# Performance work log

Measured on AMD Instinct MI355X. Metric: run time of the kernel, lower is better.

## Reference

```python
import jax, jax.numpy as jnp
import numpy as np

N, L, D = 2, 1024, 4544
H, DKV = 71, 64
ROPE_BASE = 10000.0


def _rope_tables(seq_len, head_dim, dtype):
    inv_freq = 1.0 / (ROPE_BASE ** (jnp.arange(0, head_dim, 2, dtype=jnp.float32) / head_dim))
    t = jnp.arange(seq_len, dtype=jnp.float32)
    freqs = jnp.outer(t, inv_freq)               # [L, Dkv/2]
    emb = jnp.concatenate([freqs, freqs], -1)    # [L, Dkv]
    return jnp.cos(emb).astype(dtype), jnp.sin(emb).astype(dtype)


def _apply_rotary(x, cos, sin):
    # x: [..., L, Dkv]; cos/sin: [L, Dkv] broadcast
    left, right = jnp.split(x, 2, axis=-1)
    rotated = jnp.concatenate([-right, left], axis=-1)
    return x * cos + rotated * sin


def setup_inputs() -> dict:
    key = jax.random.key(0)
    k1, k2, k3 = jax.random.split(key, 3)
    hidden_states = jax.random.normal(k1, (N, L, D), dtype=jnp.float32)
    w_qkv = jax.random.normal(k2, (D + 2 * DKV, D), dtype=jnp.float32) * (1.0 / np.sqrt(D))
    w_dense = jax.random.normal(k3, (D, D), dtype=jnp.float32) * (1.0 / np.sqrt(D))
    return {"hidden_states": hidden_states, "w_qkv": w_qkv, "w_dense": w_dense}


def reference(hidden_states, w_qkv, w_dense):
    n, l, d = hidden_states.shape
    # fused QKV projection -> [N, L, H+2, Dkv]
    fused = (hidden_states @ w_qkv.T).reshape(n, l, H + 2, DKV)
    q = fused[:, :, :-2, :]          # [N, L, H, Dkv]
    k = fused[:, :, -2, :]           # [N, L, Dkv] (single MQA kv head)
    v = fused[:, :, -1, :]           # [N, L, Dkv]

    cos, sin = _rope_tables(l, DKV, hidden_states.dtype)
    q = _apply_rotary(q, cos[:, None, :], sin[:, None, :])   # broadcast over heads
    k = _apply_rotary(k, cos, sin)

    scale = 1.0 / np.sqrt(DKV)
    # scores: [N, H, Lq, Lk]; kv head broadcast across all H query heads
    scores = jnp.einsum('nqhd,nkd->nhqk', q, k) * scale
    causal = jnp.tril(jnp.ones((l, l), dtype=bool))
    scores = jnp.where(causal, scores, jnp.finfo(scores.dtype).min)
    attn = jax.nn.softmax(scores, axis=-1)
    out = jnp.einsum('nhqk,nkd->nqhd', attn, v)              # [N, L, H, Dkv]
    out = out.reshape(n, l, H * DKV)
    return out @ w_dense.T
```

## Files before the change

### kernel.cpp

```cpp
#include <hip/hip_runtime.h>

typedef unsigned short u16;
typedef __attribute__((ext_vector_type(8))) short short8;
typedef __attribute__((ext_vector_type(4))) float floatx4;

__device__ __forceinline__ u16 f2bf(float f) {
    union { float f; unsigned int u; } v;
    v.f = f;
    unsigned int u = v.u;
    return (u16)((u + 0x7FFFu + ((u >> 16) & 1u)) >> 16);
}

__device__ __forceinline__ void cvt8_f32_bf16(const float* __restrict__ p, u16* dst) {
    const float4 x = *(const float4*)p;
    const float4 y = *(const float4*)(p + 4);
    short8 s;
    s[0] = (short)f2bf(x.x); s[1] = (short)f2bf(x.y);
    s[2] = (short)f2bf(x.z); s[3] = (short)f2bf(x.w);
    s[4] = (short)f2bf(y.x); s[5] = (short)f2bf(y.y);
    s[6] = (short)f2bf(y.z); s[7] = (short)f2bf(y.w);
    *(short8*)dst = s;
}

__device__ __forceinline__ void gld_lds16(const u16* g, u16* l) {
    __builtin_amdgcn_global_load_lds(
        (const __attribute__((address_space(1))) void*)g,
        (__attribute__((address_space(3))) void*)l,
        16, 0, 0);
}

__global__ __launch_bounds__(256) void cvt3_kernel(
    const float* __restrict__ a, u16* __restrict__ oa, long na,
    const float* __restrict__ b, u16* __restrict__ ob, long nb,
    const float* __restrict__ c, u16* __restrict__ oc, long nc) {
    const float* in; u16* out; long n;
    if (blockIdx.y == 0)      { in = a; out = oa; n = na; }
    else if (blockIdx.y == 1) { in = b; out = ob; n = nb; }
    else                      { in = c; out = oc; n = nc; }
    const long i = ((long)blockIdx.x * 256 + threadIdx.x) * 8;
    if (i >= n) return;
    cvt8_f32_bf16(in + i, out + i);
}


#define GEMM8P_PROLOGUE()                                                      \
    const int t    = threadIdx.x;                                              \
    const int w    = t >> 6;                                                   \
    const int lane = t & 63;                                                   \
    const int quad = lane >> 4;                                                \
    const int l16  = lane & 15;                                                \
    const int sw   = lane & 7;                                                 \
    const int nwg  = gridDim.x;                                                \
    const int qq = nwg >> 3, rr = nwg & 7;                                     \
    const int xcd = blockIdx.x & 7, idx = blockIdx.x >> 3;                     \
    const int wgid = (xcd < rr ? xcd * (qq + 1)                                \
                               : rr * (qq + 1) + (xcd - rr) * qq) + idx;       \
    const int m0 = (wgid / nt) * 256;                                          \
    const int n0 = (wgid % nt) * 256;                                          \
    const int wm = (w >> 2) * 128;                                             \
    const int wn = (w & 3) * 64;                                               \
    const int trow = t >> 3;                                                   \
    const int scol = ((t & 7) ^ (trow & 7)) * 8;                               \
    const long Kl = K;                                                         \
    const u16* Asrc = A + (long)(m0 + trow) * Kl + scol;                       \
    auto stageA = [&](int jt, int h, int b) {                                  \
        _Pragma("unroll")                                                      \
        for (int i = 0; i < 2; i++) {                                          \
            const u16* src = Asrc + (long)(h * 128 + i * 64) * Kl + (long)jt * 64; \
            u16* dst = &aLds[b][0] + h * 8192 + i * 4096 + t * 8;              \
            gld_lds16(src, dst);                                               \
        }                                                                      \
    };                                                                         \
    auto stageB = [&](int jt, int h, int b) {                                  \
        _Pragma("unroll")                                                      \
        for (int i = 0; i < 2; i++) {                                          \
            int rb = n0 + h * 128 + i * 64 + trow;                             \
            if (rb > N - 1) rb = N - 1;                                        \
            const u16* src = B + (long)rb * Kl + scol + (long)jt * 64;         \
            u16* dst = &bLds[b][0] + h * 8192 + i * 4096 + t * 8;              \
            gld_lds16(src, dst);                                               \
        }                                                                      \
    };                                                                         \
    floatx4 acc[8][4];                                                         \
    const floatx4 zf4 = {0.f, 0.f, 0.f, 0.f};                                  \
    _Pragma("unroll")                                                          \
    for (int i = 0; i < 8; i++)                                                \
        _Pragma("unroll")                                                      \
        for (int j = 0; j < 4; j++) acc[i][j] = zf4;                           \
                          \
    stageA(0, 0, 0); stageA(0, 1, 0);                                          \
    stageB(0, 0, 0); stageB(0, 1, 0);                                          \
    stageB(1, 0, 1); stageB(1, 1, 1);                                          \
    asm volatile("s_waitcnt vmcnt(4)" ::: "memory");                           \
    __builtin_amdgcn_s_barrier();

#define GPHASE(P, STAGE_STMT, TAIL_VM)                                         \
    {                                                                          \
        short8 afA[2], afB[2];                                                 \
        _Pragma("unroll")                                                      \
        for (int ks = 0; ks < 2; ks++) {                                       \
            afA[ks] = *(const short8*)(Ac + (wm + (2 * (P)) * 16 + l16) * 64   \
                                          + ((4 * ks + quad) ^ sw) * 8);       \
            afB[ks] = *(const short8*)(Ac + (wm + (2 * (P) + 1) * 16 + l16) * 64 \
                                          + ((4 * ks + quad) ^ sw) * 8);       \
        }                                                                      \
        STAGE_STMT;                                                            \
        __builtin_amdgcn_s_barrier();                                          \
        asm volatile("s_waitcnt lgkmcnt(0)" ::: "memory");                     \
        __builtin_amdgcn_sched_barrier(0);                                     \
        __builtin_amdgcn_s_setprio(1);                                         \
        _Pragma("unroll")                                                      \
        for (int ks = 0; ks < 2; ks++) {                                       \
            _Pragma("unroll")                                                  \
            for (int ni = 0; ni < 4; ni++) {                                   \
                acc[2 * (P)][ni] = __builtin_amdgcn_mfma_f32_16x16x32_bf16(    \
                    afA[ks], bf[ni][ks], acc[2 * (P)][ni], 0, 0, 0);           \
                acc[2 * (P) + 1][ni] = __builtin_amdgcn_mfma_f32_16x16x32_bf16(\
                    afB[ks], bf[ni][ks], acc[2 * (P) + 1][ni], 0, 0, 0);       \
            }                                                                  \
        }                                                                      \
        __builtin_amdgcn_s_setprio(0);                                         \
        TAIL_VM;                                                               \
        __builtin_amdgcn_s_barrier();                                          \
    }

#define GEMM8P_KLOOP()                                                         \
    const int JT = K >> 6;                                                     \
    for (int j = 0; j < JT; ++j) {                                             \
        const int cur = j & 1;                                                 \
        const int nb  = cur ^ 1;                                               \
        const int jn1 = (j + 1 < JT) ? j + 1 : JT - 1;                         \
        const int jn2 = (j + 2 < JT) ? j + 2 : JT - 1;                         \
        const u16* Ac = &aLds[cur][0];                                         \
        const u16* Bc = &bLds[cur][0];                                         \
        short8 bf[4][2];                                                       \
        _Pragma("unroll")                                                      \
        for (int ni = 0; ni < 4; ni++)                                         \
            _Pragma("unroll")                                                  \
            for (int ks = 0; ks < 2; ks++)                                     \
                bf[ni][ks] = *(const short8*)(Bc + (wn + ni * 16 + l16) * 64   \
                                                 + ((4 * ks + quad) ^ sw) * 8);\
        GPHASE(0, stageA(jn1, 0, nb), );                                       \
        GPHASE(1, stageA(jn1, 1, nb), );                                       \
        GPHASE(2, stageB(jn2, 0, cur), );                                      \
        GPHASE(3, stageB(jn2, 1, cur),                                         \
               asm volatile("s_waitcnt vmcnt(4)" ::: "memory"));               \
    }                                                                          \
    asm volatile("s_waitcnt vmcnt(0)" ::: "memory");

__global__ __launch_bounds__(512, 2) void gemm_qkv_8p(
    const u16* __restrict__ A, const u16* __restrict__ B,
    u16* __restrict__ qb, u16* __restrict__ kb, u16* __restrict__ vt,
    int M, int N, int K, int nt) {
    __shared__ __align__(16) u16 aLds[2][256 * 64];
    __shared__ __align__(16) u16 bLds[2][256 * 64];
    GEMM8P_PROLOGUE()
    GEMM8P_KLOOP()

#pragma unroll
    for (int ni = 0; ni < 4; ni++) {
        const int c = n0 + wn + ni * 16 + l16;
        if (c >= N) continue;
        const int hh = c >> 6;
        const int d  = c & 63;
        float inv = 0.f;
        if (hh < 72) inv = expf((float)(2 * (d & 31)) * (-0.14391156831212787f));
#pragma unroll
        for (int mi = 0; mi < 8; mi++) {
#pragma unroll
            for (int r = 0; r < 4; r++) {
                const int row = m0 + wm + mi * 16 + quad * 4 + r;
                const int tn = row >> 10;
                const int tl = row & 1023;
                float val = acc[mi][ni][r];
                if (hh < 72) {
                    float sv, cv;
                    sincosf((float)tl * inv, &sv, &cv);
                    const float pacc = acc[mi][ni ^ 2][r];
                    val = val * cv + ((d < 32) ? -pacc : pacc) * sv;
                }
                if (hh < 71) {
                    qb[((long)((tn * 71 + hh) * 1024 + tl)) * 64 + d] = f2bf(val * 0.125f);
                } else if (hh == 71) {
                    kb[((long)(tn * 1024 + tl)) * 64 + d] = f2bf(val);
                } else {
                    vt[((long)(tn * 64 + d)) * 1024 + tl] = f2bf(val);
                }
            }
        }
    }
}

__global__ __launch_bounds__(512, 2) void gemm_dense_8p(
    const u16* __restrict__ A, const u16* __restrict__ B,
    float* __restrict__ C, int M, int N, int K, int nt) {
    __shared__ __align__(16) u16 aLds[2][256 * 64];
    __shared__ __align__(16) u16 bLds[2][256 * 64];
    GEMM8P_PROLOGUE()
    GEMM8P_KLOOP()

#pragma unroll
    for (int ni = 0; ni < 4; ni++) {
        const int col = n0 + wn + ni * 16 + l16;
        if (col >= N) continue;
#pragma unroll
        for (int mi = 0; mi < 8; mi++) {
#pragma unroll
            for (int r = 0; r < 4; r++) {
                const int row = m0 + wm + mi * 16 + quad * 4 + r;
                C[(long)row * N + col] = acc[mi][ni][r];
            }
        }
    }
}

__global__ __launch_bounds__(256) void attn_kernel2(const u16* __restrict__ qb,
                                                    const u16* __restrict__ kb,
                                                    const u16* __restrict__ vt,
                                                    u16* __restrict__ ao) {
    __shared__ __align__(16) u16 k_lds[2][64 * 72];
    __shared__ __align__(16) u16 v_lds[2][64 * 72];
    __shared__ __align__(16) u16 p_lds[4][16 * 72];
    const int qt2 = blockIdx.x;
    const int h   = blockIdx.y;
    const int n   = blockIdx.z;
    const int t    = threadIdx.x;
    const int w    = t >> 6;
    const int lane = t & 63;
    const int quad = lane >> 4;
    const int l16  = lane & 15;
    const int Q0 = qt2 * 128;

    short8 aq[2][2];
#pragma unroll
    for (int mf = 0; mf < 2; mf++) {
        const u16* qrow = qb +
            ((long)((n * 71 + h) * 1024 + Q0 + 64 * mf + w * 16 + l16)) * 64;
        aq[mf][0] = *(const short8*)(qrow + quad * 8);
        aq[mf][1] = *(const short8*)(qrow + 32 + quad * 8);
    }

    floatx4 o[2][4];
    float lst[2][4];
    const floatx4 zf4 = {0.f, 0.f, 0.f, 0.f};
#pragma unroll
    for (int mf = 0; mf < 2; mf++) {
#pragma unroll
        for (int i = 0; i < 4; i++) { o[mf][i] = zf4; lst[mf][i] = 0.f; }
    }

    const int srow = t >> 2;
    const int scol = (t & 3) * 16;
    const u16* kb_n = kb + (long)n * 1024 * 64;
    const u16* vt_n = vt + (long)n * 64 * 1024;
    u16* pw = p_lds[w];

    const int ktend = 2 * qt2 + 2;

    auto stage = [&](int kt, int b) {
        const u16* krow = kb_n + (long)(kt * 64 + srow) * 64 + scol;
        *(uint4*)(k_lds[b] + srow * 72 + scol)     = *(const uint4*)(krow);
        *(uint4*)(k_lds[b] + srow * 72 + scol + 8) = *(const uint4*)(krow + 8);
        const u16* vrow = vt_n + (long)srow * 1024 + kt * 64 + scol;
        *(uint4*)(v_lds[b] + srow * 72 + scol)     = *(const uint4*)(vrow);
        *(uint4*)(v_lds[b] + srow * 72 + scol + 8) = *(const uint4*)(vrow + 8);
    };

    stage(0, 0);
    for (int kt = 0; kt < ktend; kt++) {
        const int buf = kt & 1;
        __syncthreads();
        if (kt + 1 < ktend) stage(kt + 1, 1 - buf);

#pragma unroll
        for (int mf = 0; mf < 2; mf++) {
            if (mf == 0 && kt == 2 * qt2 + 1) continue;
            floatx4 s[4];
#pragma unroll
            for (int sub = 0; sub < 4; sub++) {
                const short8 b0 = *(const short8*)(k_lds[buf] + (sub * 16 + l16) * 72 + quad * 8);
                const short8 b1 = *(const short8*)(k_lds[buf] + (sub * 16 + l16) * 72 + 32 + quad * 8);
                floatx4 z = zf4;
                z = __builtin_amdgcn_mfma_f32_16x16x32_bf16(aq[mf][0], b0, z, 0, 0, 0);
                z = __builtin_amdgcn_mfma_f32_16x16x32_bf16(aq[mf][1], b1, z, 0, 0, 0);
                s[sub] = z;
            }
            const bool diag = (kt == 2 * qt2 + mf);
            const int rowb = Q0 + 64 * mf + w * 16 + quad * 4;
#pragma unroll
            for (int sub = 0; sub < 4; sub++) {
                const int key = kt * 64 + sub * 16 + l16;
#pragma unroll
                for (int r = 0; r < 4; r++) {
                    float p = __expf(s[sub][r]);
                    if (diag && key > rowb + r) p = 0.f;
                    lst[mf][r] += p;
                    pw[(quad * 4 + r) * 72 + sub * 16 + l16] = f2bf(p);
                }
            }
            const short8 ap0 = *(const short8*)(pw + l16 * 72 + quad * 8);
            const short8 ap1 = *(const short8*)(pw + l16 * 72 + 32 + quad * 8);
#pragma unroll
            for (int dch = 0; dch < 4; dch++) {
                const short8 bv0 = *(const short8*)(v_lds[buf] + (dch * 16 + l16) * 72 + quad * 8);
                const short8 bv1 = *(const short8*)(v_lds[buf] + (dch * 16 + l16) * 72 + 32 + quad * 8);
                o[mf][dch] = __builtin_amdgcn_mfma_f32_16x16x32_bf16(ap0, bv0, o[mf][dch], 0, 0, 0);
                o[mf][dch] = __builtin_amdgcn_mfma_f32_16x16x32_bf16(ap1, bv1, o[mf][dch], 0, 0, 0);
            }
        }
    }

    float lsum[2][4];
#pragma unroll
    for (int mf = 0; mf < 2; mf++) {
#pragma unroll
        for (int r = 0; r < 4; r++) {
            float v = lst[mf][r];
#pragma unroll
            for (int mk = 1; mk < 16; mk <<= 1) v += __shfl_xor(v, mk, 64);
            lsum[mf][r] = v;
        }
    }
#pragma unroll
    for (int mf = 0; mf < 2; mf++) {
#pragma unroll
        for (int dch = 0; dch < 4; dch++) {
#pragma unroll
            for (int r = 0; r < 4; r++) {
                const float val = o[mf][dch][r] / lsum[mf][r];
                const int row = n * 1024 + Q0 + 64 * mf + w * 16 + quad * 4 + r;
                const int col = h * 64 + dch * 16 + l16;
                ao[(long)row * 4544 + col] = f2bf(val);
            }
        }
    }
}

__global__ __launch_bounds__(256) void gemm_qkv_f32(const float* __restrict__ A,
                                                    const float* __restrict__ B,
                                                    u16* __restrict__ qb,
                                                    u16* __restrict__ kb,
                                                    u16* __restrict__ vt,
                                                    int M, int N, int K) {
    __shared__ __align__(16) u16 a_lds[128 * 32];
    __shared__ __align__(16) u16 b_lds[128 * 32];
    const int t    = threadIdx.x;
    const int lane = t & 63;
    const int w    = t >> 6;
    const int quad = lane >> 4;
    const int l16  = lane & 15;
    const int m0 = blockIdx.y * 128;
    const int n0 = blockIdx.x * 128;
    const int wm = (w >> 1) * 64;
    const int wn = (w & 1) * 64;
    const int srow = t >> 2;
    const int scol = (t & 3) * 8;
    const float* Ap0 = A + (long)(m0 + srow) * K + scol;
    const float* Ap1 = A + (long)(m0 + 64 + srow) * K + scol;
    int bn0 = n0 + srow;      if (bn0 >= N) bn0 = N - 1;
    int bn1 = n0 + 64 + srow; if (bn1 >= N) bn1 = N - 1;
    const float* Bp0 = B + (long)bn0 * K + scol;
    const float* Bp1 = B + (long)bn1 * K + scol;
    u16* as0 = a_lds + srow * 32 + scol;
    u16* as1 = a_lds + (64 + srow) * 32 + scol;
    u16* bs0 = b_lds + srow * 32 + scol;
    u16* bs1 = b_lds + (64 + srow) * 32 + scol;
    floatx4 acc[4][4];
    const floatx4 zf4 = {0.f, 0.f, 0.f, 0.f};
#pragma unroll
    for (int i = 0; i < 4; i++)
#pragma unroll
        for (int j = 0; j < 4; j++) acc[i][j] = zf4;
    for (int k0 = 0; k0 < K; k0 += 32) {
        cvt8_f32_bf16(Ap0 + k0, as0);
        cvt8_f32_bf16(Ap1 + k0, as1);
        cvt8_f32_bf16(Bp0 + k0, bs0);
        cvt8_f32_bf16(Bp1 + k0, bs1);
        __syncthreads();
        short8 af[4], bfr[4];
#pragma unroll
        for (int i = 0; i < 4; i++)
            af[i] = *(const short8*)(a_lds + (wm + i * 16 + l16) * 32 + quad * 8);
#pragma unroll
        for (int j = 0; j < 4; j++)
            bfr[j] = *(const short8*)(b_lds + (wn + j * 16 + l16) * 32 + quad * 8);
#pragma unroll
        for (int i = 0; i < 4; i++)
#pragma unroll
            for (int j = 0; j < 4; j++)
                acc[i][j] = __builtin_amdgcn_mfma_f32_16x16x32_bf16(af[i], bfr[j], acc[i][j], 0, 0, 0);
        __syncthreads();
    }
#pragma unroll
    for (int j = 0; j < 4; j++) {
        const int c = n0 + wn + j * 16 + l16;
        if (c >= N) continue;
        const int hh = c >> 6;
        const int d  = c & 63;
        float inv = 0.f;
        if (hh < 72) inv = expf((float)(2 * (d & 31)) * (-0.14391156831212787f));
#pragma unroll
        for (int i = 0; i < 4; i++) {
#pragma unroll
            for (int r = 0; r < 4; r++) {
                const int row = m0 + wm + i * 16 + quad * 4 + r;
                const int tn = row >> 10;
                const int tl = row & 1023;
                float val = acc[i][j][r];
                if (hh < 72) {
                    float sv, cv;
                    sincosf((float)tl * inv, &sv, &cv);
                    const float pacc = acc[i][j ^ 2][r];
                    val = val * cv + ((d < 32) ? -pacc : pacc) * sv;
                }
                if (hh < 71) {
                    qb[((long)((tn * 71 + hh) * 1024 + tl)) * 64 + d] = f2bf(val * 0.125f);
                } else if (hh == 71) {
                    kb[((long)(tn * 1024 + tl)) * 64 + d] = f2bf(val);
                } else {
                    vt[((long)(tn * 64 + d)) * 1024 + tl] = f2bf(val);
                }
            }
        }
    }
}

__global__ __launch_bounds__(256) void gemm_dense_f32(const u16* __restrict__ A,
                                                      const float* __restrict__ B,
                                                      float* __restrict__ C,
                                                      int M, int N, int K) {
    __shared__ __align__(16) u16 a_lds[128 * 32];
    __shared__ __align__(16) u16 b_lds[128 * 32];
    const int t    = threadIdx.x;
    const int lane = t & 63;
    const int w    = t >> 6;
    const int quad = lane >> 4;
    const int l16  = lane & 15;
    const int m0 = blockIdx.y * 128;
    const int n0 = blockIdx.x * 128;
    const int wm = (w >> 1) * 64;
    const int wn = (w & 1) * 64;
    const int srow = t >> 2;
    const int scol = (t & 3) * 8;
    const u16* Ap0 = A + (long)(m0 + srow) * K + scol;
    const u16* Ap1 = A + (long)(m0 + 64 + srow) * K + scol;
    int bn0 = n0 + srow;      if (bn0 >= N) bn0 = N - 1;
    int bn1 = n0 + 64 + srow; if (bn1 >= N) bn1 = N - 1;
    const float* Bp0 = B + (long)bn0 * K + scol;
    const float* Bp1 = B + (long)bn1 * K + scol;
    u16* as0 = a_lds + srow * 32 + scol;
    u16* as1 = a_lds + (64 + srow) * 32 + scol;
    u16* bs0 = b_lds + srow * 32 + scol;
    u16* bs1 = b_lds + (64 + srow) * 32 + scol;
    floatx4 acc[4][4];
    const floatx4 zf4 = {0.f, 0.f, 0.f, 0.f};
#pragma unroll
    for (int i = 0; i < 4; i++)
#pragma unroll
        for (int j = 0; j < 4; j++) acc[i][j] = zf4;
    for (int k0 = 0; k0 < K; k0 += 32) {
        *(uint4*)as0 = *(const uint4*)(Ap0 + k0);
        *(uint4*)as1 = *(const uint4*)(Ap1 + k0);
        cvt8_f32_bf16(Bp0 + k0, bs0);
        cvt8_f32_bf16(Bp1 + k0, bs1);
        __syncthreads();
        short8 af[4], bfr[4];
#pragma unroll
        for (int i = 0; i < 4; i++)
            af[i] = *(const short8*)(a_lds + (wm + i * 16 + l16) * 32 + quad * 8);
#pragma unroll
        for (int j = 0; j < 4; j++)
            bfr[j] = *(const short8*)(b_lds + (wn + j * 16 + l16) * 32 + quad * 8);
#pragma unroll
        for (int i = 0; i < 4; i++)
#pragma unroll
            for (int j = 0; j < 4; j++)
                acc[i][j] = __builtin_amdgcn_mfma_f32_16x16x32_bf16(af[i], bfr[j], acc[i][j], 0, 0, 0);
        __syncthreads();
    }
#pragma unroll
    for (int i = 0; i < 4; i++) {
#pragma unroll
        for (int j = 0; j < 4; j++) {
            const int col = n0 + wn + j * 16 + l16;
            if (col < N) {
#pragma unroll
                for (int r = 0; r < 4; r++) {
                    const int row = m0 + wm + i * 16 + quad * 4 + r;
                    C[(long)row * N + col] = acc[i][j][r];
                }
            }
        }
    }
}

extern "C" void kernel_launch(void* const* d_in, const int* in_sizes, int n_in,
                              void* d_out, int out_size, void* d_ws, size_t ws_size,
                              hipStream_t stream) {
    (void)in_sizes; (void)n_in; (void)out_size;
    const float* hidden  = (const float*)d_in[0];
    const float* w_qkv   = (const float*)d_in[1];
    const float* w_dense = (const float*)d_in[2];
    float* out = (float*)d_out;

    const long N_HID = (long)2048 * 4544;
    const long N_QKV = (long)4672 * 4544;
    const long N_DEN = (long)4544 * 4544;
    const long N_Q   = (long)2 * 71 * 1024 * 64;
    const long N_KV  = (long)2 * 1024 * 64;
    const long N_AO  = (long)2048 * 4544;

    const size_t needA = (size_t)(N_HID + N_QKV + N_DEN + N_Q + 2 * N_KV + N_AO) * 2;

    if (ws_size >= needA) {
        u16* hid_bf  = (u16*)d_ws;
        u16* wqkv_bf = hid_bf + N_HID;
        u16* wden_bf = wqkv_bf + N_QKV;
        u16* qbuf    = wden_bf + N_DEN;
        u16* kbuf    = qbuf + N_Q;
        u16* vtbuf   = kbuf + N_KV;
        u16* aout    = vtbuf + N_KV;

        cvt3_kernel<<<dim3(10366, 3), 256, 0, stream>>>(
            hidden, hid_bf, N_HID, w_qkv, wqkv_bf, N_QKV, w_dense, wden_bf, N_DEN);
        gemm_qkv_8p<<<dim3(8 * 19), 512, 0, stream>>>(hid_bf, wqkv_bf,
                                                      qbuf, kbuf, vtbuf,
                                                      2048, 4672, 4544, 19);
        attn_kernel2<<<dim3(8, 71, 2), 256, 0, stream>>>(qbuf, kbuf, vtbuf, aout);
        gemm_dense_8p<<<dim3(8 * 18), 512, 0, stream>>>(aout, wden_bf, out,
                                                        2048, 4544, 4544, 18);
    } else {
        u16* qbuf  = (u16*)d_ws;
        u16* kbuf  = qbuf + N_Q;
        u16* vtbuf = kbuf + N_KV;
        u16* aout  = vtbuf + N_KV;
        gemm_qkv_f32<<<dim3(37, 16), 256, 0, stream>>>(hidden, w_qkv,
                                                       qbuf, kbuf, vtbuf,
                                                       2048, 4672, 4544);
        attn_kernel2<<<dim3(8, 71, 2), 256, 0, stream>>>(qbuf, kbuf, vtbuf, aout);
        gemm_dense_f32<<<dim3(36, 16), 256, 0, stream>>>(aout, w_dense, out,
                                                         2048, 4544, 4544);
    }
}
```

Measured before the change: 622.9 us.

## Overlap dense-weight conversion with QKV GEMM via extra workgroups; inline-asm LDS reads

Moves the fp32-to-bf16 conversion of w_dense out of the standalone convert kernel and into extra workgroups appended to the QKV GEMM grid. Those workgroups can fill compute units left idle by the 152-tile GEMM, hiding the conversion's memory traffic behind GEMM compute. The XCD remap now uses the GEMM tile count instead of gridDim. LDS fragment loads are also rewritten as inline ds_read_b128 asm to pin the instruction choice. The inline asm hides these loads from the compiler's dependency tracking, so correctness relies on the explicit lgkmcnt waits, and the extra workgroups may compete with GEMM tiles for CUs and bandwidth.

```diff
diff --git a/kernel.cpp b/kernel.cpp
--- a/kernel.cpp
+++ b/kernel.cpp
@@ -28,6 +28,11 @@
         (__attribute__((address_space(3))) void*)l,
         16, 0, 0);
 }
+
+#define DSR(dst, ptr)                                                          \
+    asm volatile("ds_read_b128 %0, %1"                                         \
+                 : "=v"(dst)                                                   \
+                 : "v"((unsigned)(unsigned long long)(const void*)(ptr)))
 
 __global__ __launch_bounds__(256) void cvt3_kernel(
     const float* __restrict__ a, u16* __restrict__ oa, long na,
@@ -50,8 +55,7 @@
     const int quad = lane >> 4;                                                \
     const int l16  = lane & 15;                                                \
     const int sw   = lane & 7;                                                 \
-    const int nwg  = gridDim.x;                                                \
-    const int qq = nwg >> 3, rr = nwg & 7;                                     \
+    const int qq = nwgg >> 3, rr = nwgg & 7;                                   \
     const int xcd = blockIdx.x & 7, idx = blockIdx.x >> 3;                     \
     const int wgid = (xcd < rr ? xcd * (qq + 1)                                \
                                : rr * (qq + 1) + (xcd - rr) * qq) + idx;       \
@@ -97,13 +101,10 @@
 #define GPHASE(P, STAGE_STMT, TAIL_VM)                                         \
     {                                                                          \
         short8 afA[2], afB[2];                                                 \
-        _Pragma("unroll")                                                      \
-        for (int ks = 0; ks < 2; ks++) {                                       \
-            afA[ks] = *(const short8*)(Ac + (wm + (2 * (P)) * 16 + l16) * 64   \
-                                          + ((4 * ks + quad) ^ sw) * 8);       \
-            afB[ks] = *(const short8*)(Ac + (wm + (2 * (P) + 1) * 16 + l16) * 64 \
-                                          + ((4 * ks + quad) ^ sw) * 8);       \
-        }                                                                      \
+        DSR(afA[0], Ac + (wm + (2 * (P)) * 16 + l16) * 64 + ((quad) ^ sw) * 8);\
+        DSR(afB[0], Ac + (wm + (2 * (P) + 1) * 16 + l16) * 64 + ((quad) ^ sw) * 8); \
+        DSR(afA[1], Ac + (wm + (2 * (P)) * 16 + l16) * 64 + ((4 + quad) ^ sw) * 8); \
+        DSR(afB[1], Ac + (wm + (2 * (P) + 1) * 16 + l16) * 64 + ((4 + quad) ^ sw) * 8); \
         STAGE_STMT;                                                            \
         __builtin_amdgcn_s_barrier();                                          \
         asm volatile("s_waitcnt lgkmcnt(0)" ::: "memory");                     \
@@ -138,8 +139,8 @@
         for (int ni = 0; ni < 4; ni++)                                         \
             _Pragma("unroll")                                                  \
             for (int ks = 0; ks < 2; ks++)                                     \
-                bf[ni][ks] = *(const short8*)(Bc + (wn + ni * 16 + l16) * 64   \
-                                                 + ((4 * ks + quad) ^ sw) * 8);\
+                DSR(bf[ni][ks],                                                \
+                    Bc + (wn + ni * 16 + l16) * 64 + ((4 * ks + quad) ^ sw) * 8); \
         GPHASE(0, stageA(jn1, 0, nb), );                                       \
         GPHASE(1, stageA(jn1, 1, nb), );                                       \
         GPHASE(2, stageB(jn2, 0, cur), );                                      \
@@ -151,9 +152,20 @@
 __global__ __launch_bounds__(512, 2) void gemm_qkv_8p(
     const u16* __restrict__ A, const u16* __restrict__ B,
     u16* __restrict__ qb, u16* __restrict__ kb, u16* __restrict__ vt,
-    int M, int N, int K, int nt) {
+    int M, int N, int K, int nt,
+    const float* __restrict__ cvt_src, u16* __restrict__ cvt_dst, long cvt_n) {
     __shared__ __align__(16) u16 aLds[2][256 * 64];
     __shared__ __align__(16) u16 bLds[2][256 * 64];
+    const int nwgg = (M >> 8) * nt;
+    if ((int)blockIdx.x >= nwgg) {
+        const long blockbase = (long)((int)blockIdx.x - nwgg) * 16384;
+#pragma unroll
+        for (int u = 0; u < 4; u++) {
+            const long i = blockbase + (long)u * 4096 + (long)threadIdx.x * 8;
+            if (i < cvt_n) cvt8_f32_bf16(cvt_src + i, cvt_dst + i);
+        }
+        return;
+    }
     GEMM8P_PROLOGUE()
     GEMM8P_KLOOP()
 
@@ -196,6 +208,7 @@
     float* __restrict__ C, int M, int N, int K, int nt) {
     __shared__ __align__(16) u16 aLds[2][256 * 64];
     __shared__ __align__(16) u16 bLds[2][256 * 64];
+    const int nwgg = (M >> 8) * nt;
     GEMM8P_PROLOGUE()
     GEMM8P_KLOOP()
 
@@ -521,11 +534,12 @@
         u16* vtbuf   = kbuf + N_KV;
         u16* aout    = vtbuf + N_KV;
 
-        cvt3_kernel<<<dim3(10366, 3), 256, 0, stream>>>(
+        cvt3_kernel<<<dim3(10366, 2), 256, 0, stream>>>(
             hidden, hid_bf, N_HID, w_qkv, wqkv_bf, N_QKV, w_dense, wden_bf, N_DEN);
-        gemm_qkv_8p<<<dim3(8 * 19), 512, 0, stream>>>(hid_bf, wqkv_bf,
-                                                      qbuf, kbuf, vtbuf,
-                                                      2048, 4672, 4544, 19);
+        gemm_qkv_8p<<<dim3(8 * 19 + 1261), 512, 0, stream>>>(
+            hid_bf, wqkv_bf, qbuf, kbuf, vtbuf,
+            2048, 4672, 4544, 19,
+            w_dense, wden_bf, N_DEN);
         attn_kernel2<<<dim3(8, 71, 2), 256, 0, stream>>>(qbuf, kbuf, vtbuf, aout);
         gemm_dense_8p<<<dim3(8 * 18), 512, 0, stream>>>(aout, wden_bf, out,
                                                         2048, 4544, 4544, 18);
```

New measurement: 537.2 us. 13.8% less time.
